# Optimization experiments

Measured on AMD Instinct MI355X. Metric: run time of the kernel, lower is better.

Reference implementation:

```python
import jax, jax.numpy as jnp
import numpy as np

B, C, F_, T = 32, 2, 1024, 512
CF = C * F_
H = 128  # lstm hidden / embedding dim


def setup_inputs() -> dict:
    key = jax.random.key(0)
    ks = jax.random.split(key, 12)
    s = 0.05
    return {
        "x": jax.random.normal(ks[0], (B, C, F_, T), dtype=jnp.float32),
        "W_fc1": jax.random.normal(ks[1], (H, CF), dtype=jnp.float32) * s,
        "b_fc1": jax.random.normal(ks[2], (H,), dtype=jnp.float32) * s,
        "Wih_f": jax.random.normal(ks[3], (4 * H, H), dtype=jnp.float32) * s,
        "Whh_f": jax.random.normal(ks[4], (4 * H, H), dtype=jnp.float32) * s,
        "b_f": jax.random.normal(ks[5], (4 * H,), dtype=jnp.float32) * s,
        "Wih_b": jax.random.normal(ks[6], (4 * H, H), dtype=jnp.float32) * s,
        "Whh_b": jax.random.normal(ks[7], (4 * H, H), dtype=jnp.float32) * s,
        "b_b": jax.random.normal(ks[8], (4 * H,), dtype=jnp.float32) * s,
        "W_out": jax.random.normal(ks[9], (H, 2 * H), dtype=jnp.float32) * s,
        "b_out": jax.random.normal(ks[10], (H,), dtype=jnp.float32) * s,
    }


def _lstm_scan(x, Wih, Whh, b):
    # x: (L, T, H); recurrence over L (torch treats the (B,128) input as an
    # unbatched sequence of length B), vectorized over the T frames.
    L, Tn, _ = x.shape
    Hn = Whh.shape[1]

    def step(carry, xt):
        h, c = carry  # (T, H)
        z = xt @ Wih.T + h @ Whh.T + b  # (T, 4H)
        i, f, g, o = jnp.split(z, 4, axis=-1)
        c = jax.nn.sigmoid(f) * c + jax.nn.sigmoid(i) * jnp.tanh(g)
        h = jax.nn.sigmoid(o) * jnp.tanh(c)
        return (h, c), h

    init = (jnp.zeros((Tn, Hn), x.dtype), jnp.zeros((Tn, Hn), x.dtype))
    _, hs = jax.lax.scan(step, init, x)
    return hs  # (L, T, H)


def reference(x, W_fc1, b_fc1, Wih_f, Whh_f, b_f, Wih_b, Whh_b, b_b, W_out, b_out):
    Bn, Cn, Fn, Tn = x.shape
    # fc1 applied per time frame: (B, CF, T) -> (B, T, 128)
    xr = x.reshape(Bn, Cn * Fn, Tn).transpose(0, 2, 1)
    h = jnp.einsum("btc,dc->btd", xr, W_fc1) + b_fc1
    # bidirectional LSTM over the batch axis (torch unbatched-input semantics)
    hf = _lstm_scan(h, Wih_f, Whh_f, b_f)
    hb = _lstm_scan(h[::-1], Wih_b, Whh_b, b_b)[::-1]
    hs = jnp.concatenate([hf, hb], axis=-1)  # (B, T, 256)
    out = jnp.einsum("btd,ed->bte", hs, W_out) + b_out  # (B, T, 128)
    return out.transpose(0, 2, 1)  # (B, 128, T), matching torch.stack(dim=2)
```

## Files before the change

### kernel.cpp

```cpp
#include <hip/hip_runtime.h>
#include <stdint.h>

typedef __attribute__((ext_vector_type(8))) short short8;
typedef __attribute__((ext_vector_type(4))) float floatx4;

__device__ __forceinline__ float bf16_to_f(uint16_t u) {
    union { uint32_t i; float f; } v; v.i = ((uint32_t)u) << 16; return v.f;
}
__device__ __forceinline__ uint16_t f_to_bf16(float f) {
    union { uint32_t i; float f; } v; v.f = f;
    uint32_t u = v.i;
    u += 0x7FFFu + ((u >> 16) & 1u);
    return (uint16_t)(u >> 16);
}
__device__ __forceinline__ void gload16(const void* g, void* l) {
    __builtin_amdgcn_global_load_lds(
        (const __attribute__((address_space(1))) void*)g,
        (__attribute__((address_space(3))) void*)l, 16, 0, 0);
}
__device__ __forceinline__ float rcpf(float x) { return __builtin_amdgcn_rcpf(x); }

__device__ __forceinline__ void bar_lds() {
    asm volatile("s_waitcnt lgkmcnt(0)" ::: "memory");
    __builtin_amdgcn_s_barrier();
    asm volatile("" ::: "memory");
}

#define B_  32
#define T_  512
#define CF_ 2048
#define H_  128
#define G4_ 512
#define LOG2E 1.4426950408889634f

__global__ __launch_bounds__(256) void k_cvt_all(
        const float* __restrict__ Wfc, const float* __restrict__ Wih_f,
        const float* __restrict__ Wih_b, const float* __restrict__ Whh_f,
        const float* __restrict__ Whh_b, const float* __restrict__ Wout,
        uint16_t* __restrict__ WfcB, uint16_t* __restrict__ WihB,
        uint16_t* __restrict__ WhhB, uint16_t* __restrict__ WoutB) {
    const int blk = blockIdx.x;
    const float* s; uint16_t* d; int off;
    if (blk < 256)      { s = Wfc;   d = WfcB;          off = blk; }
    else if (blk < 320) { s = Wih_f; d = WihB;          off = blk - 256; }
    else if (blk < 384) { s = Wih_b; d = WihB + 65536;  off = blk - 320; }
    else if (blk < 448) { s = Whh_f; d = WhhB;          off = blk - 384; }
    else if (blk < 512) { s = Whh_b; d = WhhB + 65536;  off = blk - 448; }
    else                { s = Wout;  d = WoutB;         off = blk - 512; }
    const int i = off * 1024 + threadIdx.x * 4;
    float4 v = *(const float4*)&s[i];
    ushort4 o;
    o.x = f_to_bf16(v.x); o.y = f_to_bf16(v.y);
    o.z = f_to_bf16(v.z); o.w = f_to_bf16(v.w);
    *(ushort4*)&d[i] = o;
}

__global__ __launch_bounds__(512) void k_fc1x(const float* __restrict__ x,
                                              const uint16_t* __restrict__ WfcB,
                                              const float* __restrict__ bfc,
                                              const uint16_t* __restrict__ WihB,
                                              const float* __restrict__ b_f,
                                              const float* __restrict__ b_b,
                                              uint16_t* __restrict__ Xp) {
    __shared__ float tile[64 * 65];
    __shared__ __align__(16) uint16_t As[8192];
    __shared__ __align__(16) uint16_t Bs[4224];
    __shared__ __align__(16) uint16_t Hs2[8432];

    const int bb = blockIdx.y, n0 = blockIdx.x * 64;
    const int tid = threadIdx.x, w = tid >> 6, l = tid & 63;
    const int lm = l & 15, lk = l >> 4;
    const float* xb = x + (size_t)bb * CF_ * T_;

    const int t4 = (tid & 15) * 4, cf_r = tid >> 4;
    const int kk = (tid & 15) * 4, t_r = tid >> 4;

    float4 xv0, xv1;
    {
        const float* p = &xb[(size_t)(0 + cf_r) * T_ + n0 + t4];
        xv0 = *(const float4*)p;
        xv1 = *(const float4*)(p + 32 * T_);
    }

    const int wmA = (w >> 1) * 32, wnA = (w & 1) * 32;
    floatx4 acc[2][2] = {};
    for (int k0 = 0; k0 < CF_; k0 += 64) {
        __syncthreads();
        tile[(t4 + 0) * 65 + cf_r] = xv0.x;
        tile[(t4 + 1) * 65 + cf_r] = xv0.y;
        tile[(t4 + 2) * 65 + cf_r] = xv0.z;
        tile[(t4 + 3) * 65 + cf_r] = xv0.w;
        tile[(t4 + 0) * 65 + cf_r + 32] = xv1.x;
        tile[(t4 + 1) * 65 + cf_r + 32] = xv1.y;
        tile[(t4 + 2) * 65 + cf_r + 32] = xv1.z;
        tile[(t4 + 3) * 65 + cf_r + 32] = xv1.w;
        gload16(WfcB + (size_t)l * CF_ + k0 + w * 8,        As + (w * 128 + l) * 8);
        gload16(WfcB + (size_t)(64 + l) * CF_ + k0 + w * 8, As + (w * 128 + 64 + l) * 8);
        __syncthreads();
        if (k0 + 64 < CF_) {
            const float* p = &xb[(size_t)(k0 + 64 + cf_r) * T_ + n0 + t4];
            xv0 = *(const float4*)p;
            xv1 = *(const float4*)(p + 32 * T_);
        }
        #pragma unroll
        for (int pass = 0; pass < 2; ++pass) {
            const int tr = t_r + pass * 32;
            ushort4 o;
            o.x = f_to_bf16(tile[tr * 65 + kk + 0]);
            o.y = f_to_bf16(tile[tr * 65 + kk + 1]);
            o.z = f_to_bf16(tile[tr * 65 + kk + 2]);
            o.w = f_to_bf16(tile[tr * 65 + kk + 3]);
            *(ushort4*)&Bs[((kk >> 3) * 66 + tr) * 8 + (kk & 7)] = o;
        }
        __syncthreads();
        short8 a[2][2], bfr[2][2];
        #pragma unroll
        for (int kf = 0; kf < 2; ++kf) {
            #pragma unroll
            for (int mf = 0; mf < 2; ++mf)
                a[mf][kf] = *(const short8*)&As[((kf * 4 + lk) * 128 + wmA + mf * 16 + lm) * 8];
            #pragma unroll
            for (int nf = 0; nf < 2; ++nf)
                bfr[nf][kf] = *(const short8*)&Bs[((kf * 4 + lk) * 66 + wnA + nf * 16 + lm) * 8];
        }
        #pragma unroll
        for (int mf = 0; mf < 2; ++mf)
            #pragma unroll
            for (int nf = 0; nf < 2; ++nf) {
                acc[mf][nf] = __builtin_amdgcn_mfma_f32_16x16x32_bf16(a[mf][0], bfr[nf][0], acc[mf][nf], 0, 0, 0);
                acc[mf][nf] = __builtin_amdgcn_mfma_f32_16x16x32_bf16(a[mf][1], bfr[nf][1], acc[mf][nf], 0, 0, 0);
            }
    }
    __syncthreads();
    #pragma unroll
    for (int mf = 0; mf < 2; ++mf) {
        const int d0 = wmA + mf * 16 + lk * 4;
        const float4 bv = *(const float4*)&bfc[d0];
        const int c = ((wmA + mf * 16) >> 3) + (lk >> 1);
        #pragma unroll
        for (int nf = 0; nf < 2; ++nf) {
            const int t = wnA + nf * 16 + lm;
            ushort4 o;
            o.x = f_to_bf16(acc[mf][nf][0] + bv.x);
            o.y = f_to_bf16(acc[mf][nf][1] + bv.y);
            o.z = f_to_bf16(acc[mf][nf][2] + bv.z);
            o.w = f_to_bf16(acc[mf][nf][3] + bv.w);
            *(ushort4*)&Hs2[(c * 66 + t) * 8 + (lk & 1) * 4] = o;
        }
    }
    __syncthreads();

    const int dirw = w >> 2;
    const int db   = dirw * B_ + bb;
    const uint16_t* Wp = WihB + (size_t)dirw * (G4_ * H_);
    const float* bi = dirw ? b_b : b_f;
    #pragma unroll
    for (int it = 0; it < 2; ++it) {
        const int gbase = (w & 3) * 64 + it * 256;
        short8 aw[4][4];
        #pragma unroll
        for (int mf = 0; mf < 4; ++mf)
            #pragma unroll
            for (int kf = 0; kf < 4; ++kf)
                aw[mf][kf] = *(const short8*)&Wp[(size_t)(gbase + mf * 16 + lm) * H_ + kf * 32 + lk * 8];
        floatx4 acc2[4][4] = {};
        #pragma unroll
        for (int nf = 0; nf < 4; ++nf) {
            short8 bbf[4];
            #pragma unroll
            for (int kf = 0; kf < 4; ++kf)
                bbf[kf] = *(const short8*)&Hs2[((kf * 4 + lk) * 66 + nf * 16 + lm) * 8];
            #pragma unroll
            for (int mf = 0; mf < 4; ++mf)
                #pragma unroll
                for (int kf = 0; kf < 4; ++kf)
                    acc2[mf][nf] = __builtin_amdgcn_mfma_f32_16x16x32_bf16(aw[mf][kf], bbf[kf], acc2[mf][nf], 0, 0, 0);
        }
        #pragma unroll
        for (int mf = 0; mf < 4; ++mf) {
            const int g0 = gbase + mf * 16 + lk * 4;
            const float4 bv = *(const float4*)&bi[g0];
            #pragma unroll
            for (int nf = 0; nf < 4; ++nf) {
                const int t = n0 + nf * 16 + lm;
                ushort4 o;
                o.x = f_to_bf16(acc2[mf][nf][0] + bv.x);
                o.y = f_to_bf16(acc2[mf][nf][1] + bv.y);
                o.z = f_to_bf16(acc2[mf][nf][2] + bv.z);
                o.w = f_to_bf16(acc2[mf][nf][3] + bv.w);
                *(ushort4*)&Xp[((size_t)db * T_ + t) * G4_ + g0] = o;
            }
        }
    }
}

__global__ __launch_bounds__(512) void k_lstm(const uint16_t* __restrict__ Xp,
                                              const uint16_t* __restrict__ WhhB,
                                              uint16_t* __restrict__ hs) {
    __shared__ __align__(16) uint16_t h_sh[2][16 * 136];
    const int dir = blockIdx.y, t0 = blockIdx.x * 16;
    const int tid = threadIdx.x, w = tid >> 6, l = tid & 63;
    const int lm = l & 15, lk = l >> 4;
    const int gcol = w * 16 + lm;
    const int tloc = lk * 4;
    const uint16_t* Wp = WhhB + dir * (G4_ * H_);

    short8 bw[4][4];
    #pragma unroll
    for (int q = 0; q < 4; ++q)
        #pragma unroll
        for (int kf = 0; kf < 4; ++kf)
            bw[q][kf] = *(const short8*)&Wp[(size_t)(q * H_ + gcol) * H_ + kf * 32 + lk * 8];

    for (int i = tid; i < 16 * 136; i += 512) h_sh[0][i] = 0;
    float c[4] = {0.f, 0.f, 0.f, 0.f};

    uint16_t xva[4][4], xvb[4][4];
    {
        const int b0 = dir ? (B_ - 1) : 0;
        const uint16_t* xp = Xp + ((size_t)(dir * B_ + b0) * T_ + t0 + tloc) * G4_;
        #pragma unroll
        for (int r = 0; r < 4; ++r)
            #pragma unroll
            for (int q = 0; q < 4; ++q)
                xva[r][q] = xp[(size_t)r * G4_ + q * H_ + gcol];
    }
    bar_lds();

    auto step = [&](int s, uint16_t (&xc)[4][4], uint16_t (&xn)[4][4], int par) {
        const int b_idx = dir ? (B_ - 1 - s) : s;
        short8 af[4];
        #pragma unroll
        for (int kf = 0; kf < 4; ++kf)
            af[kf] = *(const short8*)&h_sh[par][lm * 136 + kf * 32 + lk * 8];
        floatx4 acc[4] = {};
        #pragma unroll
        for (int q = 0; q < 4; ++q)
            #pragma unroll
            for (int kf = 0; kf < 4; ++kf)
                acc[q] = __builtin_amdgcn_mfma_f32_16x16x32_bf16(af[kf], bw[q][kf], acc[q], 0, 0, 0);
        if (s < B_ - 1) {
            const int bn = dir ? (B_ - 2 - s) : (s + 1);
            const uint16_t* xp = Xp + ((size_t)(dir * B_ + bn) * T_ + t0 + tloc) * G4_;
            #pragma unroll
            for (int r = 0; r < 4; ++r)
                #pragma unroll
                for (int q = 0; q < 4; ++q)
                    xn[r][q] = xp[(size_t)r * G4_ + q * H_ + gcol];
        }
        #pragma unroll
        for (int r = 0; r < 4; ++r) {
            float zi = acc[0][r] + bf16_to_f(xc[r][0]);
            float zf = acc[1][r] + bf16_to_f(xc[r][1]);
            float zg = acc[2][r] + bf16_to_f(xc[r][2]);
            float zo = acc[3][r] + bf16_to_f(xc[r][3]);
            float si = rcpf(1.f + __builtin_amdgcn_exp2f(-LOG2E * zi));
            float sf = rcpf(1.f + __builtin_amdgcn_exp2f(-LOG2E * zf));
            float so = rcpf(1.f + __builtin_amdgcn_exp2f(-LOG2E * zo));
            float tg = 1.f - 2.f * rcpf(1.f + __builtin_amdgcn_exp2f(2.f * LOG2E * zg));
            c[r] = sf * c[r] + si * tg;
            float tc = 1.f - 2.f * rcpf(1.f + __builtin_amdgcn_exp2f(2.f * LOG2E * c[r]));
            float hn = so * tc;
            uint16_t hb = f_to_bf16(hn);
            h_sh[par ^ 1][(tloc + r) * 136 + gcol] = hb;
            hs[((size_t)b_idx * T_ + t0 + tloc + r) * 256 + dir * H_ + gcol] = hb;
        }
        bar_lds();
    };

    for (int s2 = 0; s2 < 16; ++s2) {
        step(2 * s2,     xva, xvb, 0);
        step(2 * s2 + 1, xvb, xva, 1);
    }
}

__global__ __launch_bounds__(256) void k_outm(const uint16_t* __restrict__ WoutB,
                                              const uint16_t* __restrict__ hs,
                                              const float* __restrict__ bout,
                                              float* __restrict__ out) {
    __shared__ __align__(16) uint16_t As[4096], Bs[4096];
    const int b = blockIdx.z, m0 = blockIdx.y * 64, n0 = blockIdx.x * 64;
    const int tid = threadIdx.x, w = tid >> 6, l = tid & 63;
    const int wm = (w >> 1) * 32, wn = (w & 1) * 32;
    const int lm = l & 15, lk = l >> 4;
    const uint16_t* A = WoutB + (size_t)m0 * 256;
    const uint16_t* Bp = hs + ((size_t)b * T_ + n0) * 256;
    floatx4 acc[2][2] = {};
    const uint16_t* gA = A + (size_t)l * 256;
    const uint16_t* gB = Bp + (size_t)l * 256;
    for (int k0 = 0; k0 < 256; k0 += 64) {
        __syncthreads();
        gload16(gA + k0 + (2 * w) * 8,     As + ((2 * w) * 64 + l) * 8);
        gload16(gA + k0 + (2 * w + 1) * 8, As + ((2 * w + 1) * 64 + l) * 8);
        gload16(gB + k0 + (2 * w) * 8,     Bs + ((2 * w) * 64 + l) * 8);
        gload16(gB + k0 + (2 * w + 1) * 8, Bs + ((2 * w + 1) * 64 + l) * 8);
        __syncthreads();
        short8 a[2][2], bfr[2][2];
        #pragma unroll
        for (int kf = 0; kf < 2; ++kf) {
            #pragma unroll
            for (int mf = 0; mf < 2; ++mf)
                a[mf][kf] = *(const short8*)&As[((kf * 4 + lk) * 64 + wm + mf * 16 + lm) * 8];
            #pragma unroll
            for (int nf = 0; nf < 2; ++nf)
                bfr[nf][kf] = *(const short8*)&Bs[((kf * 4 + lk) * 64 + wn + nf * 16 + lm) * 8];
        }
        #pragma unroll
        for (int mf = 0; mf < 2; ++mf)
            #pragma unroll
            for (int nf = 0; nf < 2; ++nf) {
                acc[mf][nf] = __builtin_amdgcn_mfma_f32_16x16x32_bf16(a[mf][0], bfr[nf][0], acc[mf][nf], 0, 0, 0);
                acc[mf][nf] = __builtin_amdgcn_mfma_f32_16x16x32_bf16(a[mf][1], bfr[nf][1], acc[mf][nf], 0, 0, 0);
            }
    }
    #pragma unroll
    for (int mf = 0; mf < 2; ++mf) {
        const int e0 = m0 + wm + mf * 16 + lk * 4;
        const float4 bv = *(const float4*)&bout[e0];
        #pragma unroll
        for (int nf = 0; nf < 2; ++nf) {
            const int t = n0 + wn + nf * 16 + lm;
            out[((size_t)b * H_ + e0 + 0) * T_ + t] = acc[mf][nf][0] + bv.x;
            out[((size_t)b * H_ + e0 + 1) * T_ + t] = acc[mf][nf][1] + bv.y;
            out[((size_t)b * H_ + e0 + 2) * T_ + t] = acc[mf][nf][2] + bv.z;
            out[((size_t)b * H_ + e0 + 3) * T_ + t] = acc[mf][nf][3] + bv.w;
        }
    }
}

extern "C" void kernel_launch(void* const* d_in, const int* in_sizes, int n_in,
                              void* d_out, int out_size, void* d_ws, size_t ws_size,
                              hipStream_t stream) {
    const float* x     = (const float*)d_in[0];
    const float* Wfc   = (const float*)d_in[1];
    const float* bfc   = (const float*)d_in[2];
    const float* Wih_f = (const float*)d_in[3];
    const float* Whh_f = (const float*)d_in[4];
    const float* b_f   = (const float*)d_in[5];
    const float* Wih_b = (const float*)d_in[6];
    const float* Whh_b = (const float*)d_in[7];
    const float* b_b   = (const float*)d_in[8];
    const float* Wout  = (const float*)d_in[9];
    const float* bout  = (const float*)d_in[10];
    float* out = (float*)d_out;

    char* ws = (char*)d_ws;
    uint16_t* Xp    = (uint16_t*)(ws);
    uint16_t* hsB   = (uint16_t*)(ws + 33554432);
    uint16_t* WfcB  = (uint16_t*)(ws + 41943040);
    uint16_t* WihB  = (uint16_t*)(ws + 42467328);
    uint16_t* WhhB  = (uint16_t*)(ws + 42729472);
    uint16_t* WoutB = (uint16_t*)(ws + 42991616);

    k_cvt_all<<<dim3(544), 256, 0, stream>>>(Wfc, Wih_f, Wih_b, Whh_f, Whh_b, Wout,
                                             WfcB, WihB, WhhB, WoutB);
    k_fc1x <<<dim3(8, 32),   512, 0, stream>>>(x, WfcB, bfc, WihB, b_f, b_b, Xp);
    k_lstm <<<dim3(32, 2),   512, 0, stream>>>(Xp, WhhB, hsB);
    k_outm <<<dim3(8, 2, 32), 256, 0, stream>>>(WoutB, hsB, bout, out);
}
```

Measured before the change: 278.9 us.

## Double-buffer fc1 GEMM staging with two-deep x prefetch and async weight loads

The fc1 GEMM loop now double-buffers the transpose tile and the weight tile in LDS. It keeps x loads two iterations ahead in registers and issues the next weight tile's global-to-LDS loads before the current compute step. Barriers are swapped for lgkmcnt-only waits plus an explicit vmcnt wait, so memory latency can overlap with the MFMA work and each iteration needs one fewer barrier. This costs extra LDS per block, which may lower occupancy, and the correctness of the hand-counted vmcnt depends on how the compiler orders the loads.

```diff
diff --git a/kernel.cpp b/kernel.cpp
--- a/kernel.cpp
+++ b/kernel.cpp
@@ -62,8 +62,8 @@
                                               const float* __restrict__ b_f,
                                               const float* __restrict__ b_b,
                                               uint16_t* __restrict__ Xp) {
-    __shared__ float tile[64 * 65];
-    __shared__ __align__(16) uint16_t As[8192];
+    __shared__ float tile[2][64 * 65];
+    __shared__ __align__(16) uint16_t As[2][8192];
     __shared__ __align__(16) uint16_t Bs[4224];
     __shared__ __align__(16) uint16_t Hs2[8432];
 
@@ -75,50 +75,67 @@
     const int t4 = (tid & 15) * 4, cf_r = tid >> 4;
     const int kk = (tid & 15) * 4, t_r = tid >> 4;
 
-    float4 xv0, xv1;
-    {
-        const float* p = &xb[(size_t)(0 + cf_r) * T_ + n0 + t4];
-        xv0 = *(const float4*)p;
-        xv1 = *(const float4*)(p + 32 * T_);
-    }
-
     const int wmA = (w >> 1) * 32, wnA = (w & 1) * 32;
     floatx4 acc[2][2] = {};
-    for (int k0 = 0; k0 < CF_; k0 += 64) {
-        __syncthreads();
-        tile[(t4 + 0) * 65 + cf_r] = xv0.x;
-        tile[(t4 + 1) * 65 + cf_r] = xv0.y;
-        tile[(t4 + 2) * 65 + cf_r] = xv0.z;
-        tile[(t4 + 3) * 65 + cf_r] = xv0.w;
-        tile[(t4 + 0) * 65 + cf_r + 32] = xv1.x;
-        tile[(t4 + 1) * 65 + cf_r + 32] = xv1.y;
-        tile[(t4 + 2) * 65 + cf_r + 32] = xv1.z;
-        tile[(t4 + 3) * 65 + cf_r + 32] = xv1.w;
-        gload16(WfcB + (size_t)l * CF_ + k0 + w * 8,        As + (w * 128 + l) * 8);
-        gload16(WfcB + (size_t)(64 + l) * CF_ + k0 + w * 8, As + (w * 128 + 64 + l) * 8);
-        __syncthreads();
-        if (k0 + 64 < CF_) {
-            const float* p = &xb[(size_t)(k0 + 64 + cf_r) * T_ + n0 + t4];
-            xv0 = *(const float4*)p;
-            xv1 = *(const float4*)(p + 32 * T_);
+
+    float4 xA0, xA1, xB0, xB1;
+    {
+        const float* p = &xb[(size_t)cf_r * T_ + n0 + t4];
+        xA0 = *(const float4*)p;
+        xA1 = *(const float4*)(p + 32 * T_);
+    }
+    asm volatile("" ::: "memory");
+    gload16(WfcB + (size_t)l * CF_ + w * 8,        &As[0][(w * 128 + l) * 8]);
+    gload16(WfcB + (size_t)(64 + l) * CF_ + w * 8, &As[0][(w * 128 + 64 + l) * 8]);
+    asm volatile("" ::: "memory");
+    {
+        const float* p = &xb[(size_t)(64 + cf_r) * T_ + n0 + t4];
+        xB0 = *(const float4*)p;
+        xB1 = *(const float4*)(p + 32 * T_);
+    }
+
+    auto body = [&](int i, float4& x0, float4& x1, float* tc, uint16_t* AsCur,
+                    uint16_t* AsNxt) {
+        tc[(t4 + 0) * 65 + cf_r] = x0.x;
+        tc[(t4 + 1) * 65 + cf_r] = x0.y;
+        tc[(t4 + 2) * 65 + cf_r] = x0.z;
+        tc[(t4 + 3) * 65 + cf_r] = x0.w;
+        tc[(t4 + 0) * 65 + cf_r + 32] = x1.x;
+        tc[(t4 + 1) * 65 + cf_r + 32] = x1.y;
+        tc[(t4 + 2) * 65 + cf_r + 32] = x1.z;
+        tc[(t4 + 3) * 65 + cf_r + 32] = x1.w;
+        bar_lds();
+        {
+            const int kn = (i + 1 < 32) ? (i + 1) * 64 : 0;
+            gload16(WfcB + (size_t)l * CF_ + kn + w * 8,        AsNxt + (w * 128 + l) * 8);
+            gload16(WfcB + (size_t)(64 + l) * CF_ + kn + w * 8, AsNxt + (w * 128 + 64 + l) * 8);
+        }
+        asm volatile("" ::: "memory");
+        {
+            const int kx = (i + 2 < 32) ? (i + 2) * 64 : 0;
+            const float* p = &xb[(size_t)(kx + cf_r) * T_ + n0 + t4];
+            x0 = *(const float4*)p;
+            x1 = *(const float4*)(p + 32 * T_);
         }
         #pragma unroll
         for (int pass = 0; pass < 2; ++pass) {
             const int tr = t_r + pass * 32;
             ushort4 o;
-            o.x = f_to_bf16(tile[tr * 65 + kk + 0]);
-            o.y = f_to_bf16(tile[tr * 65 + kk + 1]);
-            o.z = f_to_bf16(tile[tr * 65 + kk + 2]);
-            o.w = f_to_bf16(tile[tr * 65 + kk + 3]);
+            o.x = f_to_bf16(tc[tr * 65 + kk + 0]);
+            o.y = f_to_bf16(tc[tr * 65 + kk + 1]);
+            o.z = f_to_bf16(tc[tr * 65 + kk + 2]);
+            o.w = f_to_bf16(tc[tr * 65 + kk + 3]);
             *(ushort4*)&Bs[((kk >> 3) * 66 + tr) * 8 + (kk & 7)] = o;
         }
-        __syncthreads();
+        asm volatile("s_waitcnt vmcnt(6)" ::: "memory");
+        bar_lds();
+        __builtin_amdgcn_sched_barrier(0);
         short8 a[2][2], bfr[2][2];
         #pragma unroll
         for (int kf = 0; kf < 2; ++kf) {
             #pragma unroll
             for (int mf = 0; mf < 2; ++mf)
-                a[mf][kf] = *(const short8*)&As[((kf * 4 + lk) * 128 + wmA + mf * 16 + lm) * 8];
+                a[mf][kf] = *(const short8*)&AsCur[((kf * 4 + lk) * 128 + wmA + mf * 16 + lm) * 8];
             #pragma unroll
             for (int nf = 0; nf < 2; ++nf)
                 bfr[nf][kf] = *(const short8*)&Bs[((kf * 4 + lk) * 66 + wnA + nf * 16 + lm) * 8];
@@ -130,8 +147,14 @@
                 acc[mf][nf] = __builtin_amdgcn_mfma_f32_16x16x32_bf16(a[mf][0], bfr[nf][0], acc[mf][nf], 0, 0, 0);
                 acc[mf][nf] = __builtin_amdgcn_mfma_f32_16x16x32_bf16(a[mf][1], bfr[nf][1], acc[mf][nf], 0, 0, 0);
             }
-    }
-    __syncthreads();
+    };
+
+    for (int ii = 0; ii < 16; ++ii) {
+        body(2 * ii,     xA0, xA1, tile[0], &As[0][0], &As[1][0]);
+        body(2 * ii + 1, xB0, xB1, tile[1], &As[1][0], &As[0][0]);
+    }
+
+    bar_lds();
     #pragma unroll
     for (int mf = 0; mf < 2; ++mf) {
         const int d0 = wmA + mf * 16 + lk * 4;
@@ -148,7 +171,7 @@
             *(ushort4*)&Hs2[(c * 66 + t) * 8 + (lk & 1) * 4] = o;
         }
     }
-    __syncthreads();
+    bar_lds();
 
     const int dirw = w >> 2;
     const int db   = dirw * B_ + bb;
```

Result: slower. 289.1 us (+3.6%).

## Pre-transpose input to bf16 in a separate kernel before fc1 GEMM

Applied to the files above, without the earlier changes.

Adds a kernel that converts x to bf16 and transposes it to (B,T,CF) layout, so the fc1 GEMM can load the B operand with direct global-to-LDS 16-byte loads instead of transposing fp32 tiles in shared memory. The fused fc1 and input-projection kernel is rewritten to consume the transposed buffer. This costs an extra full pass writing and reading about 64MB of workspace, plus an extra launch. It falls back to the old path if the workspace is too small.

```diff
diff --git a/kernel.cpp b/kernel.cpp
--- a/kernel.cpp
+++ b/kernel.cpp
@@ -55,6 +55,137 @@
     *(ushort4*)&d[i] = o;
 }
 
+__global__ __launch_bounds__(256) void k_xt(const float* __restrict__ x,
+                                            uint16_t* __restrict__ xT) {
+    __shared__ uint16_t tl[64][72];
+    const int b = blockIdx.z, cf0 = blockIdx.y * 64, t0 = blockIdx.x * 64;
+    const int tid = threadIdx.x;
+    const int t4 = (tid & 15) * 4, cfr = tid >> 4;
+    #pragma unroll
+    for (int pass = 0; pass < 4; ++pass) {
+        const int cf = cfr + pass * 16;
+        const float4 v = *(const float4*)
+            &x[(size_t)(b * CF_ + cf0 + cf) * T_ + t0 + t4];
+        tl[t4 + 0][cf] = f_to_bf16(v.x);
+        tl[t4 + 1][cf] = f_to_bf16(v.y);
+        tl[t4 + 2][cf] = f_to_bf16(v.z);
+        tl[t4 + 3][cf] = f_to_bf16(v.w);
+    }
+    __syncthreads();
+    const int tr = tid >> 2;
+    #pragma unroll
+    for (int pass = 0; pass < 2; ++pass) {
+        const int cfo = ((tid & 3) + 4 * pass) * 8;
+        *(short8*)&xT[(size_t)(b * T_ + t0 + tr) * CF_ + cf0 + cfo] =
+            *(const short8*)&tl[tr][cfo];
+    }
+}
+
+__global__ __launch_bounds__(512) void k_fc1g(const uint16_t* __restrict__ xT,
+                                              const uint16_t* __restrict__ WfcB,
+                                              const float* __restrict__ bfc,
+                                              const uint16_t* __restrict__ WihB,
+                                              const float* __restrict__ b_f,
+                                              const float* __restrict__ b_b,
+                                              uint16_t* __restrict__ Xp) {
+    __shared__ __align__(16) uint16_t As[8192];
+    __shared__ __align__(16) uint16_t Bs[4224];
+    __shared__ __align__(16) uint16_t Hs2[8432];
+
+    const int bb = blockIdx.y, n0 = blockIdx.x * 64;
+    const int tid = threadIdx.x, w = tid >> 6, l = tid & 63;
+    const int lm = l & 15, lk = l >> 4;
+    const uint16_t* xTb = xT + (size_t)bb * T_ * CF_;
+
+    const int wmA = (w >> 1) * 32, wnA = (w & 1) * 32;
+    floatx4 acc[2][2] = {};
+    for (int k0 = 0; k0 < CF_; k0 += 64) {
+        __syncthreads();
+        gload16(WfcB + (size_t)l * CF_ + k0 + w * 8,        As + (w * 128 + l) * 8);
+        gload16(WfcB + (size_t)(64 + l) * CF_ + k0 + w * 8, As + (w * 128 + 64 + l) * 8);
+        gload16(xTb + (size_t)(n0 + l) * CF_ + k0 + w * 8,  Bs + (w * 66 + l) * 8);
+        __syncthreads();
+        short8 a[2][2], bfr[2][2];
+        #pragma unroll
+        for (int kf = 0; kf < 2; ++kf) {
+            #pragma unroll
+            for (int mf = 0; mf < 2; ++mf)
+                a[mf][kf] = *(const short8*)&As[((kf * 4 + lk) * 128 + wmA + mf * 16 + lm) * 8];
+            #pragma unroll
+            for (int nf = 0; nf < 2; ++nf)
+                bfr[nf][kf] = *(const short8*)&Bs[((kf * 4 + lk) * 66 + wnA + nf * 16 + lm) * 8];
+        }
+        #pragma unroll
+        for (int mf = 0; mf < 2; ++mf)
+            #pragma unroll
+            for (int nf = 0; nf < 2; ++nf) {
+                acc[mf][nf] = __builtin_amdgcn_mfma_f32_16x16x32_bf16(a[mf][0], bfr[nf][0], acc[mf][nf], 0, 0, 0);
+                acc[mf][nf] = __builtin_amdgcn_mfma_f32_16x16x32_bf16(a[mf][1], bfr[nf][1], acc[mf][nf], 0, 0, 0);
+            }
+    }
+    __syncthreads();
+    #pragma unroll
+    for (int mf = 0; mf < 2; ++mf) {
+        const int d0 = wmA + mf * 16 + lk * 4;
+        const float4 bv = *(const float4*)&bfc[d0];
+        const int c = ((wmA + mf * 16) >> 3) + (lk >> 1);
+        #pragma unroll
+        for (int nf = 0; nf < 2; ++nf) {
+            const int t = wnA + nf * 16 + lm;
+            ushort4 o;
+            o.x = f_to_bf16(acc[mf][nf][0] + bv.x);
+            o.y = f_to_bf16(acc[mf][nf][1] + bv.y);
+            o.z = f_to_bf16(acc[mf][nf][2] + bv.z);
+            o.w = f_to_bf16(acc[mf][nf][3] + bv.w);
+            *(ushort4*)&Hs2[(c * 66 + t) * 8 + (lk & 1) * 4] = o;
+        }
+    }
+    __syncthreads();
+
+    const int dirw = w >> 2;
+    const int db   = dirw * B_ + bb;
+    const uint16_t* Wp = WihB + (size_t)dirw * (G4_ * H_);
+    const float* bi = dirw ? b_b : b_f;
+    #pragma unroll
+    for (int it = 0; it < 2; ++it) {
+        const int gbase = (w & 3) * 64 + it * 256;
+        short8 aw[4][4];
+        #pragma unroll
+        for (int mf = 0; mf < 4; ++mf)
+            #pragma unroll
+            for (int kf = 0; kf < 4; ++kf)
+                aw[mf][kf] = *(const short8*)&Wp[(size_t)(gbase + mf * 16 + lm) * H_ + kf * 32 + lk * 8];
+        floatx4 acc2[4][4] = {};
+        #pragma unroll
+        for (int nf = 0; nf < 4; ++nf) {
+            short8 bbf[4];
+            #pragma unroll
+            for (int kf = 0; kf < 4; ++kf)
+                bbf[kf] = *(const short8*)&Hs2[((kf * 4 + lk) * 66 + nf * 16 + lm) * 8];
+            #pragma unroll
+            for (int mf = 0; mf < 4; ++mf)
+                #pragma unroll
+                for (int kf = 0; kf < 4; ++kf)
+                    acc2[mf][nf] = __builtin_amdgcn_mfma_f32_16x16x32_bf16(aw[mf][kf], bbf[kf], acc2[mf][nf], 0, 0, 0);
+        }
+        #pragma unroll
+        for (int mf = 0; mf < 4; ++mf) {
+            const int g0 = gbase + mf * 16 + lk * 4;
+            const float4 bv = *(const float4*)&bi[g0];
+            #pragma unroll
+            for (int nf = 0; nf < 4; ++nf) {
+                const int t = n0 + nf * 16 + lm;
+                ushort4 o;
+                o.x = f_to_bf16(acc2[mf][nf][0] + bv.x);
+                o.y = f_to_bf16(acc2[mf][nf][1] + bv.y);
+                o.z = f_to_bf16(acc2[mf][nf][2] + bv.z);
+                o.w = f_to_bf16(acc2[mf][nf][3] + bv.w);
+                *(ushort4*)&Xp[((size_t)db * T_ + t) * G4_ + g0] = o;
+            }
+        }
+    }
+}
+
 __global__ __launch_bounds__(512) void k_fc1x(const float* __restrict__ x,
                                               const uint16_t* __restrict__ WfcB,
                                               const float* __restrict__ bfc,
@@ -345,16 +476,35 @@
     float* out = (float*)d_out;
 
     char* ws = (char*)d_ws;
-    uint16_t* Xp    = (uint16_t*)(ws);
-    uint16_t* hsB   = (uint16_t*)(ws + 33554432);
-    uint16_t* WfcB  = (uint16_t*)(ws + 41943040);
-    uint16_t* WihB  = (uint16_t*)(ws + 42467328);
-    uint16_t* WhhB  = (uint16_t*)(ws + 42729472);
-    uint16_t* WoutB = (uint16_t*)(ws + 42991616);
-
-    k_cvt_all<<<dim3(544), 256, 0, stream>>>(Wfc, Wih_f, Wih_b, Whh_f, Whh_b, Wout,
-                                             WfcB, WihB, WhhB, WoutB);
-    k_fc1x <<<dim3(8, 32),   512, 0, stream>>>(x, WfcB, bfc, WihB, b_f, b_b, Xp);
-    k_lstm <<<dim3(32, 2),   512, 0, stream>>>(Xp, WhhB, hsB);
-    k_outm <<<dim3(8, 2, 32), 256, 0, stream>>>(WoutB, hsB, bout, out);
-}
+    const size_t NEED_XT = 110166016;
+
+    if (ws_size >= NEED_XT) {
+        uint16_t* Xp    = (uint16_t*)(ws);
+        uint16_t* xT    = (uint16_t*)(ws + 33554432);
+        uint16_t* hsB   = (uint16_t*)(ws + 100663296);
+        uint16_t* WfcB  = (uint16_t*)(ws + 109051904);
+        uint16_t* WihB  = (uint16_t*)(ws + 109576192);
+        uint16_t* WhhB  = (uint16_t*)(ws + 109838336);
+        uint16_t* WoutB = (uint16_t*)(ws + 110100480);
+
+        k_cvt_all<<<dim3(544), 256, 0, stream>>>(Wfc, Wih_f, Wih_b, Whh_f, Whh_b, Wout,
+                                                 WfcB, WihB, WhhB, WoutB);
+        k_xt   <<<dim3(8, 32, 32), 256, 0, stream>>>(x, xT);
+        k_fc1g <<<dim3(8, 32),   512, 0, stream>>>(xT, WfcB, bfc, WihB, b_f, b_b, Xp);
+        k_lstm <<<dim3(32, 2),   512, 0, stream>>>(Xp, WhhB, hsB);
+        k_outm <<<dim3(8, 2, 32), 256, 0, stream>>>(WoutB, hsB, bout, out);
+    } else {
+        uint16_t* Xp    = (uint16_t*)(ws);
+        uint16_t* hsB   = (uint16_t*)(ws + 33554432);
+        uint16_t* WfcB  = (uint16_t*)(ws + 41943040);
+        uint16_t* WihB  = (uint16_t*)(ws + 42467328);
+        uint16_t* WhhB  = (uint16_t*)(ws + 42729472);
+        uint16_t* WoutB = (uint16_t*)(ws + 42991616);
+
+        k_cvt_all<<<dim3(544), 256, 0, stream>>>(Wfc, Wih_f, Wih_b, Whh_f, Whh_b, Wout,
+                                                 WfcB, WihB, WhhB, WoutB);
+        k_fc1x <<<dim3(8, 32),   512, 0, stream>>>(x, WfcB, bfc, WihB, b_f, b_b, Xp);
+        k_lstm <<<dim3(32, 2),   512, 0, stream>>>(Xp, WhhB, hsB);
+        k_outm <<<dim3(8, 2, 32), 256, 0, stream>>>(WoutB, hsB, bout, out);
+    }
+}
```

Result: slower. 325.8 us (+16.8%).

## Enlarge fc1 K-tile to 256 and load x directly into bf16 LDS layout

Applied to the files above, without the earlier changes.

The fc1 GEMM kernel now processes 256 K-elements per iteration instead of 64, which cuts the number of barrier rounds by four. The fp32 x tile is no longer staged through a padded LDS transpose. Each thread instead reads scalar column values, converts them to bf16 in registers and writes them straight into the MFMA B layout. In exchange it drops the register prefetch of the next x tile, uses more LDS, and replaces float4 loads with scalar per-lane global loads, which reduces memory-level parallelism per instruction.

```diff
diff --git a/kernel.cpp b/kernel.cpp
--- a/kernel.cpp
+++ b/kernel.cpp
@@ -55,16 +55,15 @@
     *(ushort4*)&d[i] = o;
 }
 
-__global__ __launch_bounds__(512) void k_fc1x(const float* __restrict__ x,
+__global__ __launch_bounds__(512) void k_fc1r(const float* __restrict__ x,
                                               const uint16_t* __restrict__ WfcB,
                                               const float* __restrict__ bfc,
                                               const uint16_t* __restrict__ WihB,
                                               const float* __restrict__ b_f,
                                               const float* __restrict__ b_b,
                                               uint16_t* __restrict__ Xp) {
-    __shared__ float tile[64 * 65];
-    __shared__ __align__(16) uint16_t As[8192];
-    __shared__ __align__(16) uint16_t Bs[4224];
+    __shared__ __align__(16) uint16_t As[32 * 1032];
+    __shared__ __align__(16) uint16_t Bs[32 * 66 * 8];
     __shared__ __align__(16) uint16_t Hs2[8432];
 
     const int bb = blockIdx.y, n0 = blockIdx.x * 64;
@@ -72,64 +71,47 @@
     const int lm = l & 15, lk = l >> 4;
     const float* xb = x + (size_t)bb * CF_ * T_;
 
-    const int t4 = (tid & 15) * 4, cf_r = tid >> 4;
-    const int kk = (tid & 15) * 4, t_r = tid >> 4;
-
-    float4 xv0, xv1;
-    {
-        const float* p = &xb[(size_t)(0 + cf_r) * T_ + n0 + t4];
-        xv0 = *(const float4*)p;
-        xv1 = *(const float4*)(p + 32 * T_);
-    }
-
     const int wmA = (w >> 1) * 32, wnA = (w & 1) * 32;
     floatx4 acc[2][2] = {};
-    for (int k0 = 0; k0 < CF_; k0 += 64) {
+
+    for (int kc = 0; kc < 8; ++kc) {
+        const int k0 = kc * 256;
         __syncthreads();
-        tile[(t4 + 0) * 65 + cf_r] = xv0.x;
-        tile[(t4 + 1) * 65 + cf_r] = xv0.y;
-        tile[(t4 + 2) * 65 + cf_r] = xv0.z;
-        tile[(t4 + 3) * 65 + cf_r] = xv0.w;
-        tile[(t4 + 0) * 65 + cf_r + 32] = xv1.x;
-        tile[(t4 + 1) * 65 + cf_r + 32] = xv1.y;
-        tile[(t4 + 2) * 65 + cf_r + 32] = xv1.z;
-        tile[(t4 + 3) * 65 + cf_r + 32] = xv1.w;
-        gload16(WfcB + (size_t)l * CF_ + k0 + w * 8,        As + (w * 128 + l) * 8);
-        gload16(WfcB + (size_t)(64 + l) * CF_ + k0 + w * 8, As + (w * 128 + 64 + l) * 8);
+        #pragma unroll
+        for (int j = 0; j < 4; ++j) {
+            const int c = w * 4 + j;
+            gload16(WfcB + (size_t)l * CF_ + k0 + c * 8,        As + c * 1032 + l * 8);
+            gload16(WfcB + (size_t)(64 + l) * CF_ + k0 + c * 8, As + c * 1032 + (64 + l) * 8);
+        }
+        float xr[8][4];
+        #pragma unroll
+        for (int p = 0; p < 8; ++p)
+            #pragma unroll
+            for (int i = 0; i < 4; ++i)
+                xr[p][i] = xb[(size_t)(k0 + w * 32 + p * 4 + i) * T_ + n0 + l];
+        #pragma unroll
+        for (int p = 0; p < 8; ++p) {
+            const int cf = w * 32 + p * 4;
+            ushort4 o;
+            o.x = f_to_bf16(xr[p][0]);
+            o.y = f_to_bf16(xr[p][1]);
+            o.z = f_to_bf16(xr[p][2]);
+            o.w = f_to_bf16(xr[p][3]);
+            *(ushort4*)&Bs[((cf >> 3) * 66 + l) * 8 + (cf & 7)] = o;
+        }
         __syncthreads();
-        if (k0 + 64 < CF_) {
-            const float* p = &xb[(size_t)(k0 + 64 + cf_r) * T_ + n0 + t4];
-            xv0 = *(const float4*)p;
-            xv1 = *(const float4*)(p + 32 * T_);
-        }
-        #pragma unroll
-        for (int pass = 0; pass < 2; ++pass) {
-            const int tr = t_r + pass * 32;
-            ushort4 o;
-            o.x = f_to_bf16(tile[tr * 65 + kk + 0]);
-            o.y = f_to_bf16(tile[tr * 65 + kk + 1]);
-            o.z = f_to_bf16(tile[tr * 65 + kk + 2]);
-            o.w = f_to_bf16(tile[tr * 65 + kk + 3]);
-            *(ushort4*)&Bs[((kk >> 3) * 66 + tr) * 8 + (kk & 7)] = o;
-        }
-        __syncthreads();
-        short8 a[2][2], bfr[2][2];
-        #pragma unroll
-        for (int kf = 0; kf < 2; ++kf) {
-            #pragma unroll
-            for (int mf = 0; mf < 2; ++mf)
-                a[mf][kf] = *(const short8*)&As[((kf * 4 + lk) * 128 + wmA + mf * 16 + lm) * 8];
-            #pragma unroll
-            for (int nf = 0; nf < 2; ++nf)
-                bfr[nf][kf] = *(const short8*)&Bs[((kf * 4 + lk) * 66 + wnA + nf * 16 + lm) * 8];
-        }
-        #pragma unroll
-        for (int mf = 0; mf < 2; ++mf)
-            #pragma unroll
-            for (int nf = 0; nf < 2; ++nf) {
-                acc[mf][nf] = __builtin_amdgcn_mfma_f32_16x16x32_bf16(a[mf][0], bfr[nf][0], acc[mf][nf], 0, 0, 0);
-                acc[mf][nf] = __builtin_amdgcn_mfma_f32_16x16x32_bf16(a[mf][1], bfr[nf][1], acc[mf][nf], 0, 0, 0);
-            }
+        #pragma unroll
+        for (int kf = 0; kf < 8; ++kf) {
+            const int ch = kf * 4 + lk;
+            short8 a0 = *(const short8*)&As[ch * 1032 + (wmA + lm) * 8];
+            short8 a1 = *(const short8*)&As[ch * 1032 + (wmA + 16 + lm) * 8];
+            short8 b0 = *(const short8*)&Bs[(ch * 66 + wnA + lm) * 8];
+            short8 b1 = *(const short8*)&Bs[(ch * 66 + wnA + 16 + lm) * 8];
+            acc[0][0] = __builtin_amdgcn_mfma_f32_16x16x32_bf16(a0, b0, acc[0][0], 0, 0, 0);
+            acc[0][1] = __builtin_amdgcn_mfma_f32_16x16x32_bf16(a0, b1, acc[0][1], 0, 0, 0);
+            acc[1][0] = __builtin_amdgcn_mfma_f32_16x16x32_bf16(a1, b0, acc[1][0], 0, 0, 0);
+            acc[1][1] = __builtin_amdgcn_mfma_f32_16x16x32_bf16(a1, b1, acc[1][1], 0, 0, 0);
+        }
     }
     __syncthreads();
     #pragma unroll
@@ -354,7 +336,7 @@
 
     k_cvt_all<<<dim3(544), 256, 0, stream>>>(Wfc, Wih_f, Wih_b, Whh_f, Whh_b, Wout,
                                              WfcB, WihB, WhhB, WoutB);
-    k_fc1x <<<dim3(8, 32),   512, 0, stream>>>(x, WfcB, bfc, WihB, b_f, b_b, Xp);
+    k_fc1r <<<dim3(8, 32),   512, 0, stream>>>(x, WfcB, bfc, WihB, b_f, b_b, Xp);
     k_lstm <<<dim3(32, 2),   512, 0, stream>>>(Xp, WhhB, hsB);
     k_outm <<<dim3(8, 2, 32), 256, 0, stream>>>(WoutB, hsB, bout, out);
 }
```

Result: slower. 294.2 us (+5.5%).
